# Kernel optimization log

Measured on AMD Instinct MI355X. Metric: run time of the kernel, lower is better.

## Reference

```python
import jax, jax.numpy as jnp
import numpy as np

B, S, D = 4, 4096, 64
D_MODEL = 64


def setup_inputs() -> dict:
    key = jax.random.key(0)
    kq, kk, kv, km = jax.random.split(key, 4)
    q = jax.random.normal(kq, (B, S, D), dtype=jnp.float32)
    k = jax.random.normal(kk, (B, S, D), dtype=jnp.float32)
    v = jax.random.normal(kv, (B, S, D), dtype=jnp.float32)
    mask = jax.random.uniform(km, (B, S, S), dtype=jnp.float32)
    return {"q": q, "k": k, "v": v, "mask": mask}


def reference(q, k, v, mask):
    dk = jnp.sqrt(jnp.asarray(D_MODEL, dtype=q.dtype))
    # [B,S,S] scores; multiplicative (non-additive) mask applied pre-softmax
    scaled_qk = jnp.einsum('bqd,bkd->bqk', q, k) / dk
    scaled_qk = scaled_qk * mask
    attn = jax.nn.softmax(scaled_qk, axis=-1)
    return jnp.einsum('bqk,bkd->bqd', attn, v)
```

## Files before the change

### kernel.cpp

```cpp
#include <hip/hip_runtime.h>
#include <hip/hip_bf16.h>

#define S_LEN 4096
#define DH 64
#define NBATCH 4

typedef __attribute__((ext_vector_type(8))) short bf16x8;
typedef __attribute__((ext_vector_type(4))) short bf16x4;
typedef __attribute__((ext_vector_type(4))) float f32x4;

static __device__ __forceinline__ short f2bf(float x) {
  __hip_bfloat16 h = __float2bfloat16(x);
  return *reinterpret_cast<short*>(&h);
}

#define MFMA(a, b, c) __builtin_amdgcn_mfma_f32_16x16x32_bf16((a), (b), (c), 0, 0, 0)

__global__ __launch_bounds__(256) void cvt_q_kernel(const float* __restrict__ q,
                                                    short* __restrict__ qb) {
  int i = (blockIdx.x * 256 + threadIdx.x) * 4;
  f32x4 x = *(const f32x4*)(q + i);
  bf16x4 o;
#pragma unroll
  for (int j = 0; j < 4; ++j) o[j] = f2bf(x[j]);
  *(bf16x4*)(qb + i) = o;
}

__global__ __launch_bounds__(256) void cvt_frag_kernel(const float* __restrict__ k,
                                                       const float* __restrict__ v,
                                                       short* __restrict__ kfrag,
                                                       short* __restrict__ vfrag) {
  __shared__ short kt[32][80];
  __shared__ short vt[32][80];
  const int t = threadIdx.x;
  const int b = blockIdx.x >> 7;
  const int i = blockIdx.x & 127;
  const size_t src0 = ((size_t)b * S_LEN + i * 32) * DH;
  {
    const int row = t >> 3, c0 = (t & 7) * 8;
    const f32x4 xk0 = *(const f32x4*)(k + src0 + row * DH + c0);
    const f32x4 xk1 = *(const f32x4*)(k + src0 + row * DH + c0 + 4);
    const f32x4 xv0 = *(const f32x4*)(v + src0 + row * DH + c0);
    const f32x4 xv1 = *(const f32x4*)(v + src0 + row * DH + c0 + 4);
#pragma unroll
    for (int j = 0; j < 4; ++j) {
      kt[row][c0 + j] = f2bf(xk0[j]);  kt[row][c0 + 4 + j] = f2bf(xk1[j]);
      vt[row][c0 + j] = f2bf(xv0[j]);  vt[row][c0 + 4 + j] = f2bf(xv1[j]);
    }
  }
  __syncthreads();
  const int c = t >> 6, l = t & 63;
  const size_t dst = (((size_t)(b * 128 + i) * 4 + c) * 64 + l) * 8;
  {
    const int kr = ((c >> 1) * 16) + (l & 15);
    const int d0 = ((c & 1) * 32) + (l >> 4) * 8;
    *(bf16x8*)(kfrag + dst) = *(const bf16x8*)&kt[kr][d0];
  }
  {
    bf16x8 f;
    const int col = c * 16 + (l & 15);
    const int r0 = (l >> 4) * 8;
#pragma unroll
    for (int j = 0; j < 8; ++j) f[j] = vt[r0 + j][col];
    *(bf16x8*)(vfrag + dst) = f;
  }
}

__global__ __launch_bounds__(256, 6) void fa_kernel(
    const short* __restrict__ qb, const short* __restrict__ kfrag,
    const short* __restrict__ vfrag, const float* __restrict__ mask,
    float* __restrict__ out, float* __restrict__ lsum) {
  __shared__ __align__(16) short lds_p[4][16][40];
  __shared__ float lds_O[4][16][64];
  __shared__ float lds_l[4][16];

  const int tid = threadIdx.x;
  const int w = tid >> 6;
  const int lane = tid & 63;
  const int quad = lane >> 4;
  const int n16 = lane & 15;

  const int b = blockIdx.x >> 9;
  const int rest = blockIdx.x & 511;
  const int q0 = (rest >> 1) << 4;
  const int hh = rest & 1;

  const short* qrow = qb + (size_t)(b * S_LEN + q0 + n16) * DH;
  const bf16x8 aQ0 = *(const bf16x8*)(qrow + quad * 8);
  const bf16x8 aQ1 = *(const bf16x8*)(qrow + 32 + quad * 8);

  f32x4 O0 = {0.f, 0.f, 0.f, 0.f}, O1 = O0, O2 = O0, O3 = O0;
  float lacc[4] = {0.f, 0.f, 0.f, 0.f};

  const float* mrow0 =
      mask + ((size_t)b * S_LEN + q0 + quad * 4) * S_LEN + hh * 2048;
  const short* kfb = kfrag + ((size_t)(b * 128 + hh * 64 + w) * 2048);
  const short* vfb = vfrag + ((size_t)(b * 128 + hh * 64 + w) * 2048);

  float mA[8], mB[8];

#define LOAD_MASK(DST, LK)                                    \
  {                                                           \
    const int lk_ = (LK);                                     \
    _Pragma("unroll") for (int r = 0; r < 4; ++r) {           \
      DST[r]     = mrow0[(size_t)r * S_LEN + lk_ + n16];      \
      DST[4 + r] = mrow0[(size_t)r * S_LEN + lk_ + 16 + n16]; \
    }                                                         \
  }

#define FA_STEP(MREG, SS)                                                  \
  {                                                                        \
    const short* kf = kfb + (SS) * 8192;                                   \
    const bf16x8 bk0 = *(const bf16x8*)(kf + lane * 8);                    \
    const bf16x8 bk1 = *(const bf16x8*)(kf + 512 + lane * 8);              \
    const bf16x8 bk2 = *(const bf16x8*)(kf + 1024 + lane * 8);             \
    const bf16x8 bk3 = *(const bf16x8*)(kf + 1536 + lane * 8);             \
    const short* vf = vfb + (SS) * 8192;                                   \
    const bf16x8 v0 = *(const bf16x8*)(vf + lane * 8);                     \
    const bf16x8 v1 = *(const bf16x8*)(vf + 512 + lane * 8);               \
    const bf16x8 v2 = *(const bf16x8*)(vf + 1024 + lane * 8);              \
    const bf16x8 v3 = *(const bf16x8*)(vf + 1536 + lane * 8);              \
    const f32x4 z = {0.f, 0.f, 0.f, 0.f};                                  \
    f32x4 s0 = MFMA(aQ0, bk0, z); s0 = MFMA(aQ1, bk1, s0);                 \
    f32x4 s1 = MFMA(aQ0, bk2, z); s1 = MFMA(aQ1, bk3, s1);                 \
    _Pragma("unroll") for (int r = 0; r < 4; ++r) {                        \
      float p0 = __expf(s0[r] * 0.125f * MREG[r]);                         \
      float p1 = __expf(s1[r] * 0.125f * MREG[4 + r]);                     \
      lacc[r] += p0 + p1;                                                  \
      lds_p[w][quad * 4 + r][n16] = f2bf(p0);                              \
      lds_p[w][quad * 4 + r][16 + n16] = f2bf(p1);                         \
    }                                                                      \
    const bf16x8 aP = *(const bf16x8*)(&lds_p[w][n16][quad * 8]);          \
    O0 = MFMA(aP, v0, O0); O1 = MFMA(aP, v1, O1);                          \
    O2 = MFMA(aP, v2, O2); O3 = MFMA(aP, v3, O3);                          \
  }

  LOAD_MASK(mA, w * 32);
  LOAD_MASK(mB, 128 + w * 32);

  for (int it = 0; it < 8; ++it) {
    const int s2 = it * 2;
    FA_STEP(mA, s2);
    LOAD_MASK(mA, ((s2 + 2) * 128 + w * 32) & 2047);
    FA_STEP(mB, s2 + 1);
    LOAD_MASK(mB, ((s2 + 3) * 128 + w * 32) & 2047);
  }
#undef LOAD_MASK
#undef FA_STEP

#pragma unroll
  for (int r = 0; r < 4; ++r) {
#pragma unroll
    for (int off = 1; off < 16; off <<= 1) lacc[r] += __shfl_xor(lacc[r], off);
  }

#pragma unroll
  for (int r = 0; r < 4; ++r) {
    int row = quad * 4 + r;
    lds_O[w][row][n16]      = O0[r];
    lds_O[w][row][16 + n16] = O1[r];
    lds_O[w][row][32 + n16] = O2[r];
    lds_O[w][row][48 + n16] = O3[r];
    if (n16 == 0) lds_l[w][row] = lacc[r];
  }
  __syncthreads();

  const int r = tid >> 4;
  const int c4 = (tid & 15) << 2;
  float* op = out + (size_t)(b * S_LEN + q0 + r) * DH + c4;
#pragma unroll
  for (int j = 0; j < 4; ++j)
    atomicAdd(op + j, lds_O[0][r][c4 + j] + lds_O[1][r][c4 + j] +
                          lds_O[2][r][c4 + j] + lds_O[3][r][c4 + j]);
  if (tid < 16)
    atomicAdd(lsum + (size_t)b * S_LEN + q0 + tid,
              lds_l[0][tid] + lds_l[1][tid] + lds_l[2][tid] + lds_l[3][tid]);
}

__global__ __launch_bounds__(256) void norm_kernel(float* __restrict__ out,
                                                   const float* __restrict__ lsum) {
  int i = (blockIdx.x * 256 + threadIdx.x) * 4;
  f32x4 x = *(f32x4*)(out + i);
  const float inv = 1.0f / lsum[i >> 6];
#pragma unroll
  for (int j = 0; j < 4; ++j) x[j] *= inv;
  *(f32x4*)(out + i) = x;
}

extern "C" void kernel_launch(void* const* d_in, const int* in_sizes, int n_in,
                              void* d_out, int out_size, void* d_ws, size_t ws_size,
                              hipStream_t stream) {
  const float* q = (const float*)d_in[0];
  const float* k = (const float*)d_in[1];
  const float* v = (const float*)d_in[2];
  const float* mask = (const float*)d_in[3];
  float* out = (float*)d_out;

  short* qb = (short*)d_ws;
  short* kfrag = qb + (size_t)NBATCH * S_LEN * DH;
  short* vfrag = kfrag + (size_t)NBATCH * S_LEN * DH;
  float* lsum = (float*)(vfrag + (size_t)NBATCH * S_LEN * DH);

  hipMemsetAsync(d_out, 0, (size_t)NBATCH * S_LEN * DH * sizeof(float), stream);
  hipMemsetAsync(lsum, 0, (size_t)NBATCH * S_LEN * sizeof(float), stream);

  cvt_q_kernel<<<(NBATCH * S_LEN * DH) / 1024, 256, 0, stream>>>(q, qb);
  cvt_frag_kernel<<<NBATCH * 128, 256, 0, stream>>>(k, v, kfrag, vfrag);
  fa_kernel<<<NBATCH * 512, 256, 0, stream>>>(qb, kfrag, vfrag, mask, out, lsum);
  norm_kernel<<<(NBATCH * S_LEN * DH) / 1024, 256, 0, stream>>>(out, lsum);
}
```

Baseline: 432.3 us.

## Drop key-split atomics, transpose QK^T for vectorized mask loads, prefetch K fragments

Each block now covers all 4096 keys for its 16 query rows instead of half. The atomicAdd reduction, both memsets and the separate normalization kernel go away, and the output is normalized and stored directly. The S tile is computed transposed (K as the A operand), so each lane reads its mask values as contiguous float4 loads and writes P to LDS as bf16x4 vectors. K fragments and mask values are double-buffered across steps, and block indices are swizzled across XCDs. The trade-offs are half as many blocks, a lower occupancy hint (6 to 4), and a longer serial loop per block.

```diff
diff --git a/kernel.cpp b/kernel.cpp
--- a/kernel.cpp
+++ b/kernel.cpp
@@ -66,10 +66,10 @@
   }
 }
 
-__global__ __launch_bounds__(256, 6) void fa_kernel(
+__global__ __launch_bounds__(256, 4) void fa_kernel(
     const short* __restrict__ qb, const short* __restrict__ kfrag,
     const short* __restrict__ vfrag, const float* __restrict__ mask,
-    float* __restrict__ out, float* __restrict__ lsum) {
+    float* __restrict__ out) {
   __shared__ __align__(16) short lds_p[4][16][40];
   __shared__ float lds_O[4][16][64];
   __shared__ float lds_l[4][16];
@@ -80,111 +80,108 @@
   const int quad = lane >> 4;
   const int n16 = lane & 15;
 
-  const int b = blockIdx.x >> 9;
-  const int rest = blockIdx.x & 511;
-  const int q0 = (rest >> 1) << 4;
-  const int hh = rest & 1;
+  const int vb = ((blockIdx.x & 7) << 7) | (blockIdx.x >> 3);
+  const int b = vb >> 8;
+  const int q0 = (vb & 255) << 4;
 
   const short* qrow = qb + (size_t)(b * S_LEN + q0 + n16) * DH;
   const bf16x8 aQ0 = *(const bf16x8*)(qrow + quad * 8);
   const bf16x8 aQ1 = *(const bf16x8*)(qrow + 32 + quad * 8);
 
   f32x4 O0 = {0.f, 0.f, 0.f, 0.f}, O1 = O0, O2 = O0, O3 = O0;
-  float lacc[4] = {0.f, 0.f, 0.f, 0.f};
-
-  const float* mrow0 =
-      mask + ((size_t)b * S_LEN + q0 + quad * 4) * S_LEN + hh * 2048;
-  const short* kfb = kfrag + ((size_t)(b * 128 + hh * 64 + w) * 2048);
-  const short* vfb = vfrag + ((size_t)(b * 128 + hh * 64 + w) * 2048);
-
-  float mA[8], mB[8];
-
-#define LOAD_MASK(DST, LK)                                    \
-  {                                                           \
-    const int lk_ = (LK);                                     \
-    _Pragma("unroll") for (int r = 0; r < 4; ++r) {           \
-      DST[r]     = mrow0[(size_t)r * S_LEN + lk_ + n16];      \
-      DST[4 + r] = mrow0[(size_t)r * S_LEN + lk_ + 16 + n16]; \
-    }                                                         \
-  }
-
-#define FA_STEP(MREG, SS)                                                  \
+  float lacc = 0.f;
+
+  const float* mrow = mask + ((size_t)b * S_LEN + q0 + n16) * S_LEN;
+  const short* kfb = kfrag + (size_t)(b * 128 + w) * 2048;
+  const short* vfb = vfrag + (size_t)(b * 128 + w) * 2048;
+
+  bf16x8 kA0, kA1, kA2, kA3, kB0, kB1, kB2, kB3;
+  f32x4 mA0, mA1, mB0, mB1;
+
+#define LOAD_BK(B0, B1, B2, B3, SS)                       \
+  {                                                       \
+    const short* kf_ = kfb + (size_t)(SS) * 8192;         \
+    B0 = *(const bf16x8*)(kf_ + lane * 8);                \
+    B1 = *(const bf16x8*)(kf_ + 512 + lane * 8);          \
+    B2 = *(const bf16x8*)(kf_ + 1024 + lane * 8);         \
+    B3 = *(const bf16x8*)(kf_ + 1536 + lane * 8);         \
+  }
+
+#define LOAD_MASK(D0, D1, LK)                             \
+  {                                                       \
+    const int lk_ = (LK);                                 \
+    D0 = *(const f32x4*)(mrow + lk_ + quad * 4);          \
+    D1 = *(const f32x4*)(mrow + lk_ + 16 + quad * 4);     \
+  }
+
+#define FA_STEP(B0, B1, B2, B3, M0, M1, SS)                                \
   {                                                                        \
-    const short* kf = kfb + (SS) * 8192;                                   \
-    const bf16x8 bk0 = *(const bf16x8*)(kf + lane * 8);                    \
-    const bf16x8 bk1 = *(const bf16x8*)(kf + 512 + lane * 8);              \
-    const bf16x8 bk2 = *(const bf16x8*)(kf + 1024 + lane * 8);             \
-    const bf16x8 bk3 = *(const bf16x8*)(kf + 1536 + lane * 8);             \
-    const short* vf = vfb + (SS) * 8192;                                   \
-    const bf16x8 v0 = *(const bf16x8*)(vf + lane * 8);                     \
-    const bf16x8 v1 = *(const bf16x8*)(vf + 512 + lane * 8);               \
-    const bf16x8 v2 = *(const bf16x8*)(vf + 1024 + lane * 8);              \
-    const bf16x8 v3 = *(const bf16x8*)(vf + 1536 + lane * 8);              \
+    const short* vf_ = vfb + (size_t)(SS) * 8192;                          \
+    const bf16x8 v0 = *(const bf16x8*)(vf_ + lane * 8);                    \
+    const bf16x8 v1 = *(const bf16x8*)(vf_ + 512 + lane * 8);              \
+    const bf16x8 v2 = *(const bf16x8*)(vf_ + 1024 + lane * 8);             \
+    const bf16x8 v3 = *(const bf16x8*)(vf_ + 1536 + lane * 8);             \
     const f32x4 z = {0.f, 0.f, 0.f, 0.f};                                  \
-    f32x4 s0 = MFMA(aQ0, bk0, z); s0 = MFMA(aQ1, bk1, s0);                 \
-    f32x4 s1 = MFMA(aQ0, bk2, z); s1 = MFMA(aQ1, bk3, s1);                 \
+    f32x4 s0 = MFMA(B0, aQ0, z); s0 = MFMA(B1, aQ1, s0);                   \
+    f32x4 s1 = MFMA(B2, aQ0, z); s1 = MFMA(B3, aQ1, s1);                   \
+    LOAD_BK(B0, B1, B2, B3, ((SS) + 2) & 31); \
+    float p0_[4], p1_[4];                                                  \
     _Pragma("unroll") for (int r = 0; r < 4; ++r) {                        \
-      float p0 = __expf(s0[r] * 0.125f * MREG[r]);                         \
-      float p1 = __expf(s1[r] * 0.125f * MREG[4 + r]);                     \
-      lacc[r] += p0 + p1;                                                  \
-      lds_p[w][quad * 4 + r][n16] = f2bf(p0);                              \
-      lds_p[w][quad * 4 + r][16 + n16] = f2bf(p1);                         \
+      p0_[r] = __expf(s0[r] * 0.125f * M0[r]);                             \
+      p1_[r] = __expf(s1[r] * 0.125f * M1[r]);                             \
+      lacc += p0_[r] + p1_[r];                                             \
     }                                                                      \
-    const bf16x8 aP = *(const bf16x8*)(&lds_p[w][n16][quad * 8]);          \
+    LOAD_MASK(M0, M1, (((SS) + 2) * 128 + w * 32) & 4095);   \
+    bf16x4 w0_, w1_;                                                       \
+    _Pragma("unroll") for (int r = 0; r < 4; ++r) {                        \
+      w0_[r] = f2bf(p0_[r]); w1_[r] = f2bf(p1_[r]);                        \
+    }                                                                      \
+    *(bf16x4*)&lds_p[w][n16][quad * 4] = w0_;                              \
+    *(bf16x4*)&lds_p[w][n16][16 + quad * 4] = w1_;                         \
+    const bf16x8 aP = *(const bf16x8*)&lds_p[w][n16][quad * 8];            \
     O0 = MFMA(aP, v0, O0); O1 = MFMA(aP, v1, O1);                          \
     O2 = MFMA(aP, v2, O2); O3 = MFMA(aP, v3, O3);                          \
   }
 
-  LOAD_MASK(mA, w * 32);
-  LOAD_MASK(mB, 128 + w * 32);
-
-  for (int it = 0; it < 8; ++it) {
+  LOAD_BK(kA0, kA1, kA2, kA3, 0);
+  LOAD_BK(kB0, kB1, kB2, kB3, 1);
+  LOAD_MASK(mA0, mA1, w * 32);
+  LOAD_MASK(mB0, mB1, 128 + w * 32);
+
+#pragma unroll 1
+  for (int it = 0; it < 16; ++it) {
     const int s2 = it * 2;
-    FA_STEP(mA, s2);
-    LOAD_MASK(mA, ((s2 + 2) * 128 + w * 32) & 2047);
-    FA_STEP(mB, s2 + 1);
-    LOAD_MASK(mB, ((s2 + 3) * 128 + w * 32) & 2047);
-  }
+    FA_STEP(kA0, kA1, kA2, kA3, mA0, mA1, s2);
+    FA_STEP(kB0, kB1, kB2, kB3, mB0, mB1, s2 + 1);
+  }
+#undef LOAD_BK
 #undef LOAD_MASK
 #undef FA_STEP
 
+  lacc += __shfl_xor(lacc, 16);
+  lacc += __shfl_xor(lacc, 32);
+
 #pragma unroll
   for (int r = 0; r < 4; ++r) {
-#pragma unroll
-    for (int off = 1; off < 16; off <<= 1) lacc[r] += __shfl_xor(lacc[r], off);
-  }
-
-#pragma unroll
-  for (int r = 0; r < 4; ++r) {
-    int row = quad * 4 + r;
+    const int row = quad * 4 + r;
     lds_O[w][row][n16]      = O0[r];
     lds_O[w][row][16 + n16] = O1[r];
     lds_O[w][row][32 + n16] = O2[r];
     lds_O[w][row][48 + n16] = O3[r];
-    if (n16 == 0) lds_l[w][row] = lacc[r];
-  }
+  }
+  if (lane < 16) lds_l[w][lane] = lacc;
   __syncthreads();
 
   const int r = tid >> 4;
   const int c4 = (tid & 15) << 2;
-  float* op = out + (size_t)(b * S_LEN + q0 + r) * DH + c4;
+  const float inv =
+      1.0f / (lds_l[0][r] + lds_l[1][r] + lds_l[2][r] + lds_l[3][r]);
+  f32x4 acc;
 #pragma unroll
   for (int j = 0; j < 4; ++j)
-    atomicAdd(op + j, lds_O[0][r][c4 + j] + lds_O[1][r][c4 + j] +
-                          lds_O[2][r][c4 + j] + lds_O[3][r][c4 + j]);
-  if (tid < 16)
-    atomicAdd(lsum + (size_t)b * S_LEN + q0 + tid,
-              lds_l[0][tid] + lds_l[1][tid] + lds_l[2][tid] + lds_l[3][tid]);
-}
-
-__global__ __launch_bounds__(256) void norm_kernel(float* __restrict__ out,
-                                                   const float* __restrict__ lsum) {
-  int i = (blockIdx.x * 256 + threadIdx.x) * 4;
-  f32x4 x = *(f32x4*)(out + i);
-  const float inv = 1.0f / lsum[i >> 6];
-#pragma unroll
-  for (int j = 0; j < 4; ++j) x[j] *= inv;
-  *(f32x4*)(out + i) = x;
+    acc[j] = (lds_O[0][r][c4 + j] + lds_O[1][r][c4 + j] +
+              lds_O[2][r][c4 + j] + lds_O[3][r][c4 + j]) * inv;
+  *(f32x4*)(out + (size_t)(b * S_LEN + q0 + r) * DH + c4) = acc;
 }
 
 extern "C" void kernel_launch(void* const* d_in, const int* in_sizes, int n_in,
@@ -199,13 +196,8 @@
   short* qb = (short*)d_ws;
   short* kfrag = qb + (size_t)NBATCH * S_LEN * DH;
   short* vfrag = kfrag + (size_t)NBATCH * S_LEN * DH;
-  float* lsum = (float*)(vfrag + (size_t)NBATCH * S_LEN * DH);
-
-  hipMemsetAsync(d_out, 0, (size_t)NBATCH * S_LEN * DH * sizeof(float), stream);
-  hipMemsetAsync(lsum, 0, (size_t)NBATCH * S_LEN * sizeof(float), stream);
 
   cvt_q_kernel<<<(NBATCH * S_LEN * DH) / 1024, 256, 0, stream>>>(q, qb);
   cvt_frag_kernel<<<NBATCH * 128, 256, 0, stream>>>(k, v, kfrag, vfrag);
-  fa_kernel<<<NBATCH * 512, 256, 0, stream>>>(qb, kfrag, vfrag, mask, out, lsum);
-  norm_kernel<<<(NBATCH * S_LEN * DH) / 1024, 256, 0, stream>>>(out, lsum);
-}
+  fa_kernel<<<NBATCH * 256, 256, 0, stream>>>(qb, kfrag, vfrag, mask, out);
+}
```

Result: faster. 398.5 us (-7.8%).
